# Kernel optimization log

Hardware: AMD Instinct MI355X
Metric: run time of the kernel (lower is better)

## Reference

```python
import jax, jax.numpy as jnp
import numpy as np

N_NODES = 100000
N_EDGES = 1600000
DIM = 64
BN_EPS = 1e-5


def setup_inputs() -> dict:
    key = jax.random.key(0)
    ks = jax.random.split(key, 6)
    x = jax.random.normal(ks[0], (N_NODES, DIM), dtype=jnp.float32)
    edge_index = jax.random.randint(ks[1], (2, N_EDGES), 0, N_NODES, dtype=jnp.int32)
    W = jax.random.normal(ks[2], (DIM, DIM), dtype=jnp.float32) / np.sqrt(DIM)
    b = jax.random.normal(ks[3], (DIM,), dtype=jnp.float32) * 0.01
    gamma = jnp.ones((DIM,), dtype=jnp.float32)
    beta = jnp.zeros((DIM,), dtype=jnp.float32)
    return {"x": x, "edge_index": edge_index, "W": W, "b": b, "gamma": gamma, "beta": beta}


def reference(x, edge_index, W, b, gamma, beta):
    n = x.shape[0]
    src, dst = edge_index[0], edge_index[1]
    # GCNConv adds self loops
    loop = jnp.arange(n, dtype=edge_index.dtype)
    src = jnp.concatenate([src, loop])
    dst = jnp.concatenate([dst, loop])
    # symmetric degree normalization: D^-1/2 (A+I) D^-1/2
    deg = jax.ops.segment_sum(jnp.ones(src.shape[0], x.dtype), dst, num_segments=n)
    dinv = jnp.where(deg > 0, jax.lax.rsqrt(deg), 0.0)
    norm = dinv[src] * dinv[dst]  # [E+N]
    h = x @ W  # [N, D] transform before aggregation (GCN order)
    msg = h[src] * norm[:, None]  # gather + scale
    out = jax.ops.segment_sum(msg, dst, num_segments=n) + b  # scatter-add
    # BatchNorm1d (training mode: batch statistics, biased variance)
    mean = jnp.mean(out, axis=0)
    var = jnp.mean(jnp.square(out - mean), axis=0)
    out = (out - mean) * jax.lax.rsqrt(var + BN_EPS) * gamma + beta
    # ReLU; dropout is identity in eval mode
    return jax.nn.relu(out)
```

## Files before the change

kernel.cpp:

```cpp
#include <hip/hip_runtime.h>

#define N_NODES 100000
#define N_EDGES 1600000
#define DIM 64
#define BN_EPS 1e-5f

#define BNODES 128
#define NBUCK ((N_NODES + BNODES - 1) / BNODES)
#define CAP_RAW 2560
#define CAP_OUT 3584
#define TILE 4096
#define ABLK ((N_EDGES + TILE - 1) / TILE)

#define GBLK 6250

typedef __bf16 bf16x8 __attribute__((ext_vector_type(8)));
typedef float floatx4 __attribute__((ext_vector_type(4)));

static __device__ __forceinline__ unsigned short f2bf(float f) {
    unsigned u = __float_as_uint(f);
    u = (u + 0x7FFFu + ((u >> 16) & 1u)) >> 16;
    return (unsigned short)u;
}
static __device__ __forceinline__ float bf2f(unsigned short h) {
    return __uint_as_float(((unsigned)h) << 16);
}

__global__ void __launch_bounds__(1024)
passA_kernel(const int* __restrict__ src, const int* __restrict__ dst,
             int* __restrict__ cur, unsigned int* __restrict__ entries, int E) {
    __shared__ int hist[NBUCK];
    __shared__ int lbase[NBUCK];
    int t = threadIdx.x;
    if (t < NBUCK) hist[t] = 0;
    __syncthreads();

    int e0   = blockIdx.x * TILE;
    int eend = min(e0 + TILE, E);
    int eb   = e0 + t * 4;

    int dreg[4], sreg[4], ne = 0;
    if (eb + 3 < eend) {
        int4 d4 = *(const int4*)(dst + eb);
        int4 s4 = *(const int4*)(src + eb);
        dreg[0] = d4.x; dreg[1] = d4.y; dreg[2] = d4.z; dreg[3] = d4.w;
        sreg[0] = s4.x; sreg[1] = s4.y; sreg[2] = s4.z; sreg[3] = s4.w;
        ne = 4;
    } else {
        for (int e = eb; e < eend && ne < 4; ++e, ++ne) {
            dreg[ne] = dst[e];
            sreg[ne] = src[e];
        }
    }
#pragma unroll
    for (int k = 0; k < 4; ++k)
        if (k < ne) atomicAdd(&hist[dreg[k] >> 7], 1);
    __syncthreads();
    if (t < NBUCK) {
        int ii = t + (blockIdx.x * 331) % NBUCK;
        if (ii >= NBUCK) ii -= NBUCK;
        int c = hist[ii];
        lbase[ii] = (c > 0) ? atomicAdd(&cur[ii], c) : 0;
        hist[ii] = 0;
    }
    __syncthreads();
#pragma unroll
    for (int k = 0; k < 4; ++k) {
        if (k >= ne) break;
        int s = sreg[k];
        int d = dreg[k];
        int b = d >> 7;
        int r = atomicAdd(&hist[b], 1);
        int pos = lbase[b] + r;
        if (pos < CAP_RAW)
            entries[(size_t)b * CAP_OUT + pos] = ((unsigned)s << 7) | (unsigned)(d & 127);
    }
}

__global__ void __launch_bounds__(256)
build_kernel(unsigned int* __restrict__ entries, const int* __restrict__ cur,
             int* __restrict__ rowbeg, int* __restrict__ rowend,
             float* __restrict__ dinv,
             const float* __restrict__ x, const float* __restrict__ W,
             unsigned short* __restrict__ hb, int dummyIdx, int N) {
    __shared__ unsigned int raw[CAP_RAW];
    __shared__ int hist[BNODES * 4];
    __shared__ int sbuf[BNODES];
    __shared__ int nstart[BNODES];
    __shared__ int cursor[BNODES * 4];
    __shared__ float sdinv[BNODES];
    int bucket = blockIdx.x;
    int t = threadIdx.x;
    int node0 = bucket * BNODES;
    int nn = min(BNODES, N - node0);
    int cnt = min(cur[bucket], CAP_RAW);
    unsigned int* eb = entries + (size_t)bucket * CAP_OUT;

    for (int i = t; i < BNODES * 4; i += 256) hist[i] = 0;
    __syncthreads();
    for (int i = t; i < cnt; i += 256) {
        unsigned int e = eb[i];
        raw[i] = e;
        int s = (int)(e >> 7);
        int q = (s >= 25000) + (s >= 50000) + (s >= 75000);
        atomicAdd(&hist[((e & 127) << 2) | q], 1);
    }
    __syncthreads();
    int deg_t = 0, pdeg_t = 0;
    if (t < BNODES) {
        deg_t = hist[t * 4] + hist[t * 4 + 1] + hist[t * 4 + 2] + hist[t * 4 + 3];
        pdeg_t = (deg_t + 7) & ~7;
        sbuf[t] = pdeg_t;
    }
    __syncthreads();
    for (int off = 1; off < BNODES; off <<= 1) {
        int add = (t < BNODES && t >= off) ? sbuf[t - off] : 0;
        __syncthreads();
        if (t < BNODES) sbuf[t] += add;
        __syncthreads();
    }
    if (t < BNODES) {
        int ex = sbuf[t] - pdeg_t;
        nstart[t] = ex;
        int o = ex;
        cursor[t * 4 + 0] = o; o += hist[t * 4 + 0];
        cursor[t * 4 + 1] = o; o += hist[t * 4 + 1];
        cursor[t * 4 + 2] = o; o += hist[t * 4 + 2];
        cursor[t * 4 + 3] = o;
    }
    __syncthreads();
    for (int i = t; i < cnt; i += 256) {
        unsigned int e = raw[i];
        int s = (int)(e >> 7);
        int q = (s >= 25000) + (s >= 50000) + (s >= 75000);
        int p = atomicAdd(&cursor[((e & 127) << 2) | q], 1);
        eb[p] = (unsigned)s;
    }
    if (t < nn) {
        int dg  = deg_t;
        int pdg = pdeg_t;
        int base = nstart[t];
        for (int k = dg; k < pdg; ++k) eb[base + k] = (unsigned)dummyIdx;
        int gbase = bucket * CAP_OUT + base;
        rowbeg[node0 + t] = gbase;
        rowend[node0 + t] = gbase + pdg;
        float di = rsqrtf((float)(dg + 1));
        dinv[node0 + t] = di;
        sdinv[t] = di;
    }
    __syncthreads();

    int lane = t & 63, wv = t >> 6;
    int m = lane & 15, quad = lane >> 4;
    int nchunk = nn >> 4;
    bf16x8 bfrag[2][4];
#pragma unroll
    for (int c = 0; c < 2; ++c)
#pragma unroll
        for (int nt = 0; nt < 4; ++nt) {
            bf16x8 f;
#pragma unroll
            for (int j = 0; j < 8; ++j) {
                int k = c * 32 + quad * 8 + j;
                f[j] = (__bf16)W[k * DIM + nt * 16 + m];
            }
            bfrag[c][nt] = f;
        }
    for (int c2 = wv; c2 < nchunk; c2 += 4) {
        int lrow0 = c2 * 16;
        int row0 = node0 + lrow0;
        const float* xr = x + (size_t)(row0 + m) * DIM;
        bf16x8 afrag[2];
#pragma unroll
        for (int c = 0; c < 2; ++c) {
            float4 lo = *(const float4*)(xr + c * 32 + quad * 8);
            float4 hi = *(const float4*)(xr + c * 32 + quad * 8 + 4);
            bf16x8 f;
            f[0] = (__bf16)lo.x; f[1] = (__bf16)lo.y; f[2] = (__bf16)lo.z; f[3] = (__bf16)lo.w;
            f[4] = (__bf16)hi.x; f[5] = (__bf16)hi.y; f[6] = (__bf16)hi.z; f[7] = (__bf16)hi.w;
            afrag[c] = f;
        }
        float dv = sdinv[lrow0 + m];
#pragma unroll
        for (int nt = 0; nt < 4; ++nt) {
            floatx4 acc = {0.f, 0.f, 0.f, 0.f};
            acc = __builtin_amdgcn_mfma_f32_16x16x32_bf16(bfrag[0][nt], afrag[0], acc, 0, 0, 0);
            acc = __builtin_amdgcn_mfma_f32_16x16x32_bf16(bfrag[1][nt], afrag[1], acc, 0, 0, 0);
            ushort4 pk;
            pk.x = f2bf(acc[0] * dv);
            pk.y = f2bf(acc[1] * dv);
            pk.z = f2bf(acc[2] * dv);
            pk.w = f2bf(acc[3] * dv);
            *(ushort4*)(hb + (size_t)(row0 + m) * DIM + nt * 16 + quad * 4) = pk;
        }
    }
}

__global__ void __launch_bounds__(256)
gather_kernel(const int* __restrict__ rowbeg, const int* __restrict__ rowend,
              const unsigned int* __restrict__ srt, const unsigned short* __restrict__ hb,
              const float* __restrict__ dinv, unsigned short* __restrict__ hbout,
              float* __restrict__ partial, int N) {
    __shared__ float red[2][4][64];
    int lane = threadIdx.x & 63;
    int wv   = threadIdx.x >> 6;
    int g    = blockIdx.x * 4 + wv;
    int n0   = g << 2;
    float s_sum = 0.f, s_sq = 0.f;

    if (n0 < N) {
        int beg = __builtin_amdgcn_readfirstlane(rowbeg[n0]);
        int s1  = __builtin_amdgcn_readfirstlane(rowbeg[n0 + 1]);
        int s2  = __builtin_amdgcn_readfirstlane(rowbeg[n0 + 2]);
        int s3  = __builtin_amdgcn_readfirstlane(rowbeg[n0 + 3]);
        int end = __builtin_amdgcn_readfirstlane(rowend[n0 + 3]);
        float acc0 = 0.f, acc1 = 0.f, acc2 = 0.f, acc3 = 0.f;

        for (int base = beg; base < end; base += 64) {
            int idx = base + lane;
            unsigned int sv = (idx < end) ? srt[idx] : 0u;
            int cn = min(64, end - base);
            int j = 0;
            for (; j + 16 <= cn; j += 16) {
                int pA = base + j;
                int pB = pA + 8;
                int kA = (pA >= s1) + (pA >= s2) + (pA >= s3);
                int kB = (pB >= s1) + (pB >= s2) + (pB >= s3);
                float v[16];
#pragma unroll
                for (int u = 0; u < 16; ++u) {
                    unsigned int s = (unsigned)__builtin_amdgcn_readlane((int)sv, j + u);
                    v[u] = bf2f(hb[(size_t)s * DIM + lane]);
                }
                float cA = ((v[0] + v[1]) + (v[2] + v[3])) +
                           ((v[4] + v[5]) + (v[6] + v[7]));
                float cB = ((v[8] + v[9]) + (v[10] + v[11])) +
                           ((v[12] + v[13]) + (v[14] + v[15]));
                acc0 += (kA == 0) ? cA : 0.f;
                acc1 += (kA == 1) ? cA : 0.f;
                acc2 += (kA == 2) ? cA : 0.f;
                acc3 += (kA == 3) ? cA : 0.f;
                acc0 += (kB == 0) ? cB : 0.f;
                acc1 += (kB == 1) ? cB : 0.f;
                acc2 += (kB == 2) ? cB : 0.f;
                acc3 += (kB == 3) ? cB : 0.f;
            }
            for (; j < cn; j += 8) {
                int p0 = base + j;
                int k = (p0 >= s1) + (p0 >= s2) + (p0 >= s3);
                float v[8];
#pragma unroll
                for (int u = 0; u < 8; ++u) {
                    unsigned int s = (unsigned)__builtin_amdgcn_readlane((int)sv, j + u);
                    v[u] = bf2f(hb[(size_t)s * DIM + lane]);
                }
                float csum = ((v[0] + v[1]) + (v[2] + v[3])) +
                             ((v[4] + v[5]) + (v[6] + v[7]));
                acc0 += (k == 0) ? csum : 0.f;
                acc1 += (k == 1) ? csum : 0.f;
                acc2 += (k == 2) ? csum : 0.f;
                acc3 += (k == 3) ? csum : 0.f;
            }
        }

        float v0 = (acc0 + bf2f(hb[(size_t)(n0 + 0) * DIM + lane])) * dinv[n0 + 0];
        float v1 = (acc1 + bf2f(hb[(size_t)(n0 + 1) * DIM + lane])) * dinv[n0 + 1];
        float v2 = (acc2 + bf2f(hb[(size_t)(n0 + 2) * DIM + lane])) * dinv[n0 + 2];
        float v3 = (acc3 + bf2f(hb[(size_t)(n0 + 3) * DIM + lane])) * dinv[n0 + 3];
        unsigned short r0 = f2bf(v0), r1 = f2bf(v1), r2 = f2bf(v2), r3 = f2bf(v3);
        hbout[(size_t)(n0 + 0) * DIM + lane] = r0;
        hbout[(size_t)(n0 + 1) * DIM + lane] = r1;
        hbout[(size_t)(n0 + 2) * DIM + lane] = r2;
        hbout[(size_t)(n0 + 3) * DIM + lane] = r3;
        float w0 = bf2f(r0), w1 = bf2f(r1), w2 = bf2f(r2), w3 = bf2f(r3);
        s_sum = ((w0 + w1) + (w2 + w3));
        s_sq  = ((w0 * w0 + w1 * w1) + (w2 * w2 + w3 * w3));
    }

    red[0][wv][lane] = s_sum;
    red[1][wv][lane] = s_sq;
    __syncthreads();
    if (threadIdx.x < 64) {
        int c = threadIdx.x;
        partial[(size_t)blockIdx.x * 128 + c] =
            red[0][0][c] + red[0][1][c] + red[0][2][c] + red[0][3][c];
        partial[(size_t)blockIdx.x * 128 + 64 + c] =
            red[1][0][c] + red[1][1][c] + red[1][2][c] + red[1][3][c];
    }
}

__global__ void reduce2_kernel(const float* __restrict__ partial, float* __restrict__ gstat) {
    __shared__ float buf[256];
    int t = threadIdx.x;
    int col = t & 127;
    int half = t >> 7;
    int r0 = blockIdx.x * 125;
    float acc = 0.f;
    for (int r = r0 + half; r < r0 + 125; r += 2)
        acc += partial[(size_t)r * 128 + col];
    buf[t] = acc;
    __syncthreads();
    if (t < 128) atomicAdd(&gstat[t], buf[t] + buf[t + 128]);
}

__global__ void __launch_bounds__(256)
finish_kernel(const ushort4* __restrict__ hbo, float4* __restrict__ out,
              const float* __restrict__ gstat,
              const float* __restrict__ gamma, const float* __restrict__ beta,
              int total4, int N) {
    __shared__ float scale[64];
    __shared__ float shift[64];
    int t = threadIdx.x;
    if (t < 64) {
        float invN = 1.0f / (float)N;
        float mean = gstat[t] * invN;
        float var  = gstat[64 + t] * invN - mean * mean;
        float sc   = gamma[t] * rsqrtf(var + BN_EPS);
        scale[t] = sc;
        shift[t] = beta[t] - mean * sc;
    }
    __syncthreads();
    int i = blockIdx.x * blockDim.x + t;
    if (i >= total4) return;
    int c = (i * 4) & 63;
    ushort4 u = hbo[i];
    float4 v;
    float a0 = fmaf(bf2f(u.x), scale[c],     shift[c]);
    float a1 = fmaf(bf2f(u.y), scale[c + 1], shift[c + 1]);
    float a2 = fmaf(bf2f(u.z), scale[c + 2], shift[c + 2]);
    float a3 = fmaf(bf2f(u.w), scale[c + 3], shift[c + 3]);
    v.x = a0 > 0.f ? a0 : 0.f;
    v.y = a1 > 0.f ? a1 : 0.f;
    v.z = a2 > 0.f ? a2 : 0.f;
    v.w = a3 > 0.f ? a3 : 0.f;
    out[i] = v;
}

extern "C" void kernel_launch(void* const* d_in, const int* in_sizes, int n_in,
                              void* d_out, int out_size, void* d_ws, size_t ws_size,
                              hipStream_t stream) {
    const float* x     = (const float*)d_in[0];
    const int*   eidx  = (const int*)d_in[1];
    const float* W     = (const float*)d_in[2];
    const float* gamma = (const float*)d_in[4];
    const float* beta  = (const float*)d_in[5];
    float* out = (float*)d_out;

    const int N = N_NODES;
    const int total = N * DIM;

    const int* src = eidx;
    const int* dst = eidx + N_EDGES;

    char* ws = (char*)d_ws;
    size_t off_hb      = 0;
    size_t off_hbout   = off_hb + (size_t)N * DIM * 2;
    size_t off_dinv    = off_hbout + (size_t)N * DIM * 2;
    size_t off_rowbeg  = off_dinv + (size_t)N * 4;
    size_t off_rowend  = off_rowbeg + (size_t)N * 4;
    size_t off_entries = off_rowend + (size_t)N * 4;
    size_t off_partial = off_entries + (size_t)NBUCK * CAP_OUT * 4;
    size_t off_z       = off_partial + (size_t)GBLK * 128 * 4;

    unsigned short* hb     = (unsigned short*)(ws + off_hb);
    unsigned short* hbout  = (unsigned short*)(ws + off_hbout);
    float*          dinv   = (float*)(ws + off_dinv);
    int*            rowbeg = (int*)(ws + off_rowbeg);
    int*            rowend = (int*)(ws + off_rowend);
    unsigned int*   entries = (unsigned int*)(ws + off_entries);
    float*          partial = (float*)(ws + off_partial);
    int*   cur   = (int*)(ws + off_z + 128);
    float* gstat = (float*)(cur + NBUCK);
    int dummyIdx = (int)(off_z / (DIM * 2));

    size_t zbytes = 128 + (size_t)NBUCK * 4 + 512;
    hipMemsetAsync(ws + off_z, 0, zbytes, stream);

    passA_kernel<<<ABLK, 1024, 0, stream>>>(src, dst, cur, entries, N_EDGES);

    build_kernel<<<NBUCK, 256, 0, stream>>>(entries, cur, rowbeg, rowend, dinv,
                                            x, W, hb, dummyIdx, N);

    gather_kernel<<<GBLK, 256, 0, stream>>>(rowbeg, rowend, entries, hb, dinv,
                                            hbout, partial, N);

    reduce2_kernel<<<50, 256, 0, stream>>>(partial, gstat);

    finish_kernel<<<(total / 4 + 255) / 256, 256, 0, stream>>>((const ushort4*)hbout,
                                                               (float4*)out, gstat,
                                                               gamma, beta, total / 4, N);
}
```

Before: 191.0 us.

## Fold BN stat reduction into gather via replicated atomics; prefetch next edge indices

Drops the separate reduce2 kernel and the per-block partial buffer. Each gather block now atomically adds its column sums and squares into one of 32 replicated stat slots, and every finish block sums those replicas itself. The gather loop also software-prefetches the next 64 source indices while the current chunk is processed. This removes one launch and a partials round-trip, in exchange for atomic contention, nondeterministic float summation order, and a barrier inside a divergent branch in finish.

After: 173.9 us. 9.0% less time.

```diff
diff --git a/kernel.cpp b/kernel.cpp
--- a/kernel.cpp
+++ b/kernel.cpp
@@ -13,6 +13,7 @@
 #define ABLK ((N_EDGES + TILE - 1) / TILE)
 
 #define GBLK 6250
+#define NREP 32
 
 typedef __bf16 bf16x8 __attribute__((ext_vector_type(8)));
 typedef float floatx4 __attribute__((ext_vector_type(4)));
@@ -200,7 +201,7 @@
 gather_kernel(const int* __restrict__ rowbeg, const int* __restrict__ rowend,
               const unsigned int* __restrict__ srt, const unsigned short* __restrict__ hb,
               const float* __restrict__ dinv, unsigned short* __restrict__ hbout,
-              float* __restrict__ partial, int N) {
+              float* __restrict__ gstatRep, int N) {
     __shared__ float red[2][4][64];
     int lane = threadIdx.x & 63;
     int wv   = threadIdx.x >> 6;
@@ -216,9 +217,10 @@
         int end = __builtin_amdgcn_readfirstlane(rowend[n0 + 3]);
         float acc0 = 0.f, acc1 = 0.f, acc2 = 0.f, acc3 = 0.f;
 
+        unsigned int sv = (beg + lane < end) ? srt[beg + lane] : 0u;
         for (int base = beg; base < end; base += 64) {
-            int idx = base + lane;
-            unsigned int sv = (idx < end) ? srt[idx] : 0u;
+            int nidx = base + 64 + lane;
+            unsigned int sv_next = (nidx < end) ? srt[nidx] : 0u;
             int cn = min(64, end - base);
             int j = 0;
             for (; j + 16 <= cn; j += 16) {
@@ -261,6 +263,7 @@
                 acc2 += (k == 2) ? csum : 0.f;
                 acc3 += (k == 3) ? csum : 0.f;
             }
+            sv = sv_next;
         }
 
         float v0 = (acc0 + bf2f(hb[(size_t)(n0 + 0) * DIM + lane])) * dinv[n0 + 0];
@@ -280,44 +283,44 @@
     red[0][wv][lane] = s_sum;
     red[1][wv][lane] = s_sq;
     __syncthreads();
-    if (threadIdx.x < 64) {
-        int c = threadIdx.x;
-        partial[(size_t)blockIdx.x * 128 + c] =
-            red[0][0][c] + red[0][1][c] + red[0][2][c] + red[0][3][c];
-        partial[(size_t)blockIdx.x * 128 + 64 + c] =
-            red[1][0][c] + red[1][1][c] + red[1][2][c] + red[1][3][c];
-    }
-}
-
-__global__ void reduce2_kernel(const float* __restrict__ partial, float* __restrict__ gstat) {
-    __shared__ float buf[256];
-    int t = threadIdx.x;
-    int col = t & 127;
-    int half = t >> 7;
-    int r0 = blockIdx.x * 125;
-    float acc = 0.f;
-    for (int r = r0 + half; r < r0 + 125; r += 2)
-        acc += partial[(size_t)r * 128 + col];
-    buf[t] = acc;
-    __syncthreads();
-    if (t < 128) atomicAdd(&gstat[t], buf[t] + buf[t + 128]);
+    if (threadIdx.x < 128) {
+        int c = threadIdx.x & 63;
+        int which = threadIdx.x >> 6;
+        float v = red[which][0][c] + red[which][1][c] + red[which][2][c] + red[which][3][c];
+        float* dst = gstatRep + (size_t)(blockIdx.x & (NREP - 1)) * 128 + which * 64 + c;
+        atomicAdd(dst, v);
+    }
 }
 
 __global__ void __launch_bounds__(256)
 finish_kernel(const ushort4* __restrict__ hbo, float4* __restrict__ out,
-              const float* __restrict__ gstat,
+              const float* __restrict__ gstatRep,
               const float* __restrict__ gamma, const float* __restrict__ beta,
               int total4, int N) {
     __shared__ float scale[64];
     __shared__ float shift[64];
     int t = threadIdx.x;
-    if (t < 64) {
-        float invN = 1.0f / (float)N;
-        float mean = gstat[t] * invN;
-        float var  = gstat[64 + t] * invN - mean * mean;
-        float sc   = gamma[t] * rsqrtf(var + BN_EPS);
-        scale[t] = sc;
-        shift[t] = beta[t] - mean * sc;
+    if (t < 128) {
+        int c = t & 63;
+        int which = t >> 6;
+        float acc = 0.f;
+#pragma unroll
+        for (int r = 0; r < NREP; ++r)
+            acc += gstatRep[(size_t)r * 128 + which * 64 + c];
+        red_store:;
+        __shared__ float stat[128];
+        stat[t] = acc;
+        __syncthreads();
+        if (t < 64) {
+            float invN = 1.0f / (float)N;
+            float mean = stat[t] * invN;
+            float var  = stat[64 + t] * invN - mean * mean;
+            float sc   = gamma[t] * rsqrtf(var + BN_EPS);
+            scale[t] = sc;
+            shift[t] = beta[t] - mean * sc;
+        }
+    } else {
+        __syncthreads();
     }
     __syncthreads();
     int i = blockIdx.x * blockDim.x + t;
@@ -359,8 +362,7 @@
     size_t off_rowbeg  = off_dinv + (size_t)N * 4;
     size_t off_rowend  = off_rowbeg + (size_t)N * 4;
     size_t off_entries = off_rowend + (size_t)N * 4;
-    size_t off_partial = off_entries + (size_t)NBUCK * CAP_OUT * 4;
-    size_t off_z       = off_partial + (size_t)GBLK * 128 * 4;
+    size_t off_z       = off_entries + (size_t)NBUCK * CAP_OUT * 4;
 
     unsigned short* hb     = (unsigned short*)(ws + off_hb);
     unsigned short* hbout  = (unsigned short*)(ws + off_hbout);
@@ -368,12 +370,11 @@
     int*            rowbeg = (int*)(ws + off_rowbeg);
     int*            rowend = (int*)(ws + off_rowend);
     unsigned int*   entries = (unsigned int*)(ws + off_entries);
-    float*          partial = (float*)(ws + off_partial);
-    int*   cur   = (int*)(ws + off_z + 128);
-    float* gstat = (float*)(cur + NBUCK);
+    int*   cur      = (int*)(ws + off_z + 128);
+    float* gstatRep = (float*)(cur + NBUCK);
     int dummyIdx = (int)(off_z / (DIM * 2));
 
-    size_t zbytes = 128 + (size_t)NBUCK * 4 + 512;
+    size_t zbytes = 128 + (size_t)NBUCK * 4 + (size_t)NREP * 128 * 4;
     hipMemsetAsync(ws + off_z, 0, zbytes, stream);
 
     passA_kernel<<<ABLK, 1024, 0, stream>>>(src, dst, cur, entries, N_EDGES);
@@ -382,11 +383,9 @@
                                             x, W, hb, dummyIdx, N);
 
     gather_kernel<<<GBLK, 256, 0, stream>>>(rowbeg, rowend, entries, hb, dinv,
-                                            hbout, partial, N);
-
-    reduce2_kernel<<<50, 256, 0, stream>>>(partial, gstat);
+                                            hbout, gstatRep, N);
 
     finish_kernel<<<(total / 4 + 255) / 256, 256, 0, stream>>>((const ushort4*)hbout,
-                                                               (float4*)out, gstat,
+                                                               (float4*)out, gstatRep,
                                                                gamma, beta, total / 4, N);
 }
```
